# Performance work log

Hardware: AMD Instinct MI355X
Metric: run time of the kernel (lower is better)

The kernel has to match this reference:

```python
import jax, jax.numpy as jnp
import numpy as np

B, T, C = 4, 2048, 1024
H = 16
DH = C // H  # 64


def setup_inputs() -> dict:
    key = jax.random.key(0)
    ks = jax.random.split(key, 6)
    s = 1.0 / np.sqrt(C)
    x = jax.random.normal(ks[0], (B, T, C), dtype=jnp.float32)
    # per-head projection weights, stacked: (H, C, DH)
    Wq = jax.random.uniform(ks[1], (H, C, DH), dtype=jnp.float32, minval=-s, maxval=s)
    Wk = jax.random.uniform(ks[2], (H, C, DH), dtype=jnp.float32, minval=-s, maxval=s)
    Wv = jax.random.uniform(ks[3], (H, C, DH), dtype=jnp.float32, minval=-s, maxval=s)
    # output projection (torch Linear: y = x @ W.T + b); store as (C, C) for x @ Wo
    Wo = jax.random.uniform(ks[4], (C, C), dtype=jnp.float32, minval=-s, maxval=s)
    bo = jax.random.uniform(ks[5], (C,), dtype=jnp.float32, minval=-s, maxval=s)
    return {"x": x, "Wq": Wq, "Wk": Wk, "Wv": Wv, "Wo": Wo, "bo": bo}


def reference(x, Wq, Wk, Wv, Wo, bo):
    # x: (B,T,C) -> q,k,v: (B,H,T,DH)
    q = jnp.einsum('btc,hcd->bhtd', x, Wq)
    k = jnp.einsum('btc,hcd->bhtd', x, Wk)
    v = jnp.einsum('btc,hcd->bhtd', x, Wv)
    scale = DH ** -0.5
    scores = jnp.einsum('bhtd,bhsd->bhts', q, k) * scale  # (B,H,T,T)
    causal = jnp.tril(jnp.ones((T, T), dtype=bool))
    scores = jnp.where(causal, scores, -jnp.inf)
    wei = jax.nn.softmax(scores, axis=-1)
    out = jnp.einsum('bhts,bhsd->bhtd', wei, v)  # (B,H,T,DH)
    # concat heads: (B,T,H*DH) = (B,T,C)
    out = out.transpose(0, 2, 1, 3).reshape(B, T, C)
    return out @ Wo + bo
```

## Files before the change

kernel.cpp:

```cpp
#include <hip/hip_runtime.h>

#define T_SEQ 2048
#define C_DIM 1024
#define H_NUM 16
#define DHD   64
#define B_NUM 4
#define M_ROWS (B_NUM*T_SEQ)

typedef __bf16 bf16x8 __attribute__((ext_vector_type(8)));
typedef float  f32x4  __attribute__((ext_vector_type(4)));
typedef unsigned short ushort8 __attribute__((ext_vector_type(8)));
typedef unsigned short ushort4e __attribute__((ext_vector_type(4)));

__device__ __forceinline__ unsigned short f2b(float f){
  return __builtin_bit_cast(unsigned short, (__bf16)f);
}
__device__ __forceinline__ bf16x8 as_bf(ushort8 u){ return __builtin_bit_cast(bf16x8, u); }
__device__ __forceinline__ float exp2fast(float x){ return __builtin_amdgcn_exp2f(x); }

__device__ __forceinline__ void gload16(const void* g, void* l){
  __builtin_amdgcn_global_load_lds(
      (const __attribute__((address_space(1))) void*)g,
      (__attribute__((address_space(3))) void*)l, 16, 0, 0);
}

#define MF(a,b,c) __builtin_amdgcn_mfma_f32_16x16x32_bf16(a,b,c,0,0,0)

__global__ __launch_bounds__(256) void k_conv_x(const float* __restrict__ x,
                                                unsigned short* __restrict__ xb){
  int i = blockIdx.x*256 + threadIdx.x;
  float4 f = ((const float4*)x)[i];
  ushort4e o;
  o[0]=f2b(f.x); o[1]=f2b(f.y); o[2]=f2b(f.z); o[3]=f2b(f.w);
  ((ushort4e*)xb)[i] = o;
}

__global__ __launch_bounds__(256) void k_pack_w(const float* __restrict__ wq,
                                                const float* __restrict__ wk,
                                                const float* __restrict__ wv,
                                                const float* __restrict__ wo,
                                                unsigned short* __restrict__ wt,
                                                unsigned short* __restrict__ wot){
  int idx = blockIdx.x*256 + threadIdx.x;
  if (idx < 3*C_DIM*C_DIM){
    int nall = idx >> 10; int c = idx & 1023;
    int m = nall >> 10;   int n = nall & 1023;
    int h = n >> 6, d = n & 63;
    const float* w = (m==0) ? wq : (m==1) ? wk : wv;
    float f = w[((size_t)h*C_DIM + c)*DHD + d];
    if (m == 0) f *= 0.125f * 1.4426950408889634f;
    wt[idx] = f2b(f);
  } else {
    int j = idx - 3*C_DIM*C_DIM;
    int n = j >> 10, c = j & 1023;
    wot[j] = f2b(wo[(size_t)c*C_DIM + n]);
  }
}

__global__ __launch_bounds__(256) void k_gemm_qkv(const unsigned short* __restrict__ xb,
                                                  const unsigned short* __restrict__ wt,
                                                  unsigned short* __restrict__ qo,
                                                  unsigned short* __restrict__ ko,
                                                  unsigned short* __restrict__ vo){
  __shared__ __align__(16) unsigned short a_lds[128*64];
  __shared__ __align__(16) unsigned short b_lds[128*64];
  const int tid = threadIdx.x, lane = tid & 63, wid = tid >> 6;
  const int g = lane >> 4, tl = lane & 15;
  const int wr = wid >> 1, wc = wid & 1;
  const int id = blockIdx.x;
  const int swz = (id & 7)*192 + (id >> 3);
  const int mbase = (swz / 24) * 128, nbase = (swz % 24) * 128;
  f32x4 acc[4][4] = {};
  for (int kk = 0; kk < C_DIM; kk += 64){
    __syncthreads();
    #pragma unroll
    for (int i = 0; i < 4; i++){
      const int brow = (wid*4 + i)*8;
      const int row  = brow + (lane >> 3);
      const int jj   = (lane & 7) ^ (row & 7);
      gload16(&xb[(size_t)(mbase+row)*C_DIM + kk + jj*8], &a_lds[brow*64]);
      gload16(&wt[(size_t)(nbase+row)*C_DIM + kk + jj*8], &b_lds[brow*64]);
    }
    __syncthreads();
    bf16x8 aF[4][2], bF[4][2];
    #pragma unroll
    for (int mb = 0; mb < 4; mb++){
      const int row = wr*64 + mb*16 + tl; const int s7 = row & 7;
      aF[mb][0] = as_bf(*(const ushort8*)&a_lds[row*64 + ((g     ^ s7)*8)]);
      aF[mb][1] = as_bf(*(const ushort8*)&a_lds[row*64 + (((4+g) ^ s7)*8)]);
    }
    #pragma unroll
    for (int nb = 0; nb < 4; nb++){
      const int row = wc*64 + nb*16 + tl; const int s7 = row & 7;
      bF[nb][0] = as_bf(*(const ushort8*)&b_lds[row*64 + ((g     ^ s7)*8)]);
      bF[nb][1] = as_bf(*(const ushort8*)&b_lds[row*64 + (((4+g) ^ s7)*8)]);
    }
    #pragma unroll
    for (int mb = 0; mb < 4; mb++)
      #pragma unroll
      for (int nb = 0; nb < 4; nb++){
        acc[mb][nb] = MF(aF[mb][0], bF[nb][0], acc[mb][nb]);
        acc[mb][nb] = MF(aF[mb][1], bF[nb][1], acc[mb][nb]);
      }
  }
  #pragma unroll
  for (int mb = 0; mb < 4; mb++){
    #pragma unroll
    for (int nb = 0; nb < 4; nb++){
      #pragma unroll
      for (int r = 0; r < 4; r++){
        int gr = mbase + wr*64 + mb*16 + g*4 + r;
        int gc = nbase + wc*64 + nb*16 + tl;
        int b = gr >> 11, t = gr & 2047;
        int sel = gc >> 10, nw = gc & 1023;
        int h = nw >> 6, d = nw & 63;
        unsigned short* dst = (sel == 0) ? qo : (sel == 1) ? ko : vo;
        dst[(((size_t)(b*H_NUM + h))*T_SEQ + t)*DHD + d] = f2b(acc[mb][nb][r]);
      }
    }
  }
}

__global__ __launch_bounds__(256) void k_tr_v(const unsigned short* __restrict__ vsrc,
                                              unsigned short* __restrict__ vdst){
  __shared__ __align__(16) unsigned short vr[64][72];
  int tid = threadIdx.x;
  int bh = blockIdx.y; int tbase = blockIdx.x * 64;
  const unsigned short* vb = vsrc + (size_t)bh * T_SEQ * DHD;
  unsigned short* vo = vdst + (size_t)bh * DHD * T_SEQ;
  #pragma unroll
  for (int i = 0; i < 2; i++){
    int id = tid + i*256;
    int row = id >> 3, c8 = (id & 7) << 3;
    *(ushort8*)&vr[row][c8 ^ ((row >> 3) << 3)] =
        *(const ushort8*)&vb[(size_t)(tbase + row)*DHD + c8];
  }
  __syncthreads();
  #pragma unroll
  for (int i = 0; i < 2; i++){
    int id = tid + i*256;
    int d = id >> 3, oc = id & 7;
    ushort8 out;
    #pragma unroll
    for (int j = 0; j < 8; j++){
      int t = oc*8 + j;
      out[j] = vr[t][d ^ (oc << 3)];
    }
    *(ushort8*)&vo[(size_t)d*T_SEQ + tbase + oc*8] = out;
  }
}

__global__ __launch_bounds__(512) void k_flash(const unsigned short* __restrict__ q,
                                               const unsigned short* __restrict__ k,
                                               const unsigned short* __restrict__ vtg,
                                               unsigned short* __restrict__ o){
  __shared__ __align__(16) unsigned short kbufs[2][64*64];
  __shared__ __align__(16) unsigned short vbufs[2][64*64];
  __shared__ __align__(16) unsigned short pl[8][32][72];
  const int tid = threadIdx.x, lane = tid & 63, w = tid >> 6;
  const int g = lane >> 4, tl = lane & 15;
  const int id = blockIdx.x;
  const int swz = (id & 7)*32 + (id >> 3);
  const int bh = swz >> 2, bx = swz & 3;
  const int b = bh >> 4, h = bh & 15;
  const unsigned short* qb = q   + (size_t)bh * T_SEQ * DHD;
  const unsigned short* kb = k   + (size_t)bh * T_SEQ * DHD;
  const unsigned short* vb = vtg + (size_t)bh * (size_t)DHD * T_SEQ;
  const int lrow = lane >> 3, lj = lane & 7;

  for (int pass = 0; pass < 2; ++pass){
    const int qt = pass ? (7 - bx) : bx;
    const int tbase = qt * 256;
    const int trow0 = tbase + w * 32;
    const int tmax = trow0 + 31;
    bf16x8 qF[2][2];
    #pragma unroll
    for (int tf = 0; tf < 2; tf++)
      #pragma unroll
      for (int ks = 0; ks < 2; ks++)
        qF[tf][ks] = as_bf(*(const ushort8*)&qb[(size_t)(trow0 + tf*16 + tl)*DHD + ks*32 + g*8]);
    f32x4 acc[2][4] = {};
    float mreg[2] = {-1e30f, -1e30f}, lreg[2] = {0.f, 0.f};
    const int nkt = 4*qt + 4;
    {
      const int row = w*8 + lrow;
      const int jj = lj ^ (row & 7);
      gload16(&kb[(size_t)row*DHD + jj*8],   &kbufs[0][w*8*64]);
      gload16(&vb[(size_t)row*T_SEQ + jj*8], &vbufs[0][w*8*64]);
    }
    __syncthreads();
    for (int kti = 0; kti < nkt; ++kti){
      const int cur = kti & 1;
      const int kbase = kti * 64;
      if (kti + 1 < nkt){
        const int kb2 = kbase + 64;
        const int row = w*8 + lrow;
        const int jj = lj ^ (row & 7);
        gload16(&kb[(size_t)(kb2+row)*DHD + jj*8],   &kbufs[cur^1][w*8*64]);
        gload16(&vb[(size_t)row*T_SEQ + kb2 + jj*8], &vbufs[cur^1][w*8*64]);
      }
      if (kbase <= tmax){
        const unsigned short* kcur = kbufs[cur];
        const unsigned short* vcur = vbufs[cur];
        const int s7 = tl & 7;
        f32x4 st[2][4] = {};
        __builtin_amdgcn_s_setprio(1);
        #pragma unroll
        for (int sf = 0; sf < 4; sf++){
          const int row = sf*16 + tl;
          bf16x8 kf0 = as_bf(*(const ushort8*)&kcur[row*64 + ((g     ^ s7)*8)]);
          bf16x8 kf1 = as_bf(*(const ushort8*)&kcur[row*64 + (((4+g) ^ s7)*8)]);
          #pragma unroll
          for (int tf = 0; tf < 2; tf++){
            st[tf][sf] = MF(kf0, qF[tf][0], st[tf][sf]);
            st[tf][sf] = MF(kf1, qF[tf][1], st[tf][sf]);
          }
        }
        __builtin_amdgcn_s_setprio(0);
        if (kbase + 63 > trow0){
          #pragma unroll
          for (int tf = 0; tf < 2; tf++){
            int tg = trow0 + tf*16 + tl;
            #pragma unroll
            for (int sf = 0; sf < 4; sf++)
              #pragma unroll
              for (int r = 0; r < 4; r++)
                if (kbase + sf*16 + g*4 + r > tg) st[tf][sf][r] = -1e30f;
          }
        }
        #pragma unroll
        for (int tf = 0; tf < 2; tf++){
          float mloc = -1e30f;
          #pragma unroll
          for (int sf = 0; sf < 4; sf++)
            #pragma unroll
            for (int r = 0; r < 4; r++) mloc = fmaxf(mloc, st[tf][sf][r]);
          if (__any(mloc > mreg[tf] + 8.f)){
            float mrow = fmaxf(mloc, __shfl_xor(mloc, 16));
            mrow = fmaxf(mrow, __shfl_xor(mrow, 32));
            float mnew = fmaxf(mreg[tf], mrow);
            float alpha = exp2fast(mreg[tf] - mnew);
            mreg[tf] = mnew;
            lreg[tf] *= alpha;
            #pragma unroll
            for (int df = 0; df < 4; df++)
              #pragma unroll
              for (int r = 0; r < 4; r++) acc[tf][df][r] *= alpha;
          }
          float sum = 0.f;
          #pragma unroll
          for (int sf = 0; sf < 4; sf++){
            ushort4e pk;
            #pragma unroll
            for (int r = 0; r < 4; r++){
              float p = exp2fast(st[tf][sf][r] - mreg[tf]);
              sum += p;
              pk[r] = f2b(p);
            }
            *(ushort4e*)&pl[w][tf*16 + tl][sf*16 + g*4] = pk;
          }
          lreg[tf] += sum;
        }
        bf16x8 pa[2][2];
        #pragma unroll
        for (int tf = 0; tf < 2; tf++)
          #pragma unroll
          for (int ks = 0; ks < 2; ks++)
            pa[tf][ks] = as_bf(*(const ushort8*)&pl[w][tf*16 + tl][ks*32 + g*8]);
        __builtin_amdgcn_s_setprio(1);
        #pragma unroll
        for (int df = 0; df < 4; df++){
          const int row = df*16 + tl;
          bf16x8 vf0 = as_bf(*(const ushort8*)&vcur[row*64 + ((g     ^ s7)*8)]);
          bf16x8 vf1 = as_bf(*(const ushort8*)&vcur[row*64 + (((4+g) ^ s7)*8)]);
          #pragma unroll
          for (int tf = 0; tf < 2; tf++){
            acc[tf][df] = MF(vf0, pa[tf][0], acc[tf][df]);
            acc[tf][df] = MF(vf1, pa[tf][1], acc[tf][df]);
          }
        }
        __builtin_amdgcn_s_setprio(0);
      }
      __syncthreads();
    }
    #pragma unroll
    for (int tf = 0; tf < 2; tf++){
      float l = lreg[tf];
      l += __shfl_xor(l, 16);
      l += __shfl_xor(l, 32);
      float inv = 1.f / l;
      int tg = trow0 + tf*16 + tl;
      #pragma unroll
      for (int df = 0; df < 4; df++){
        ushort4e ov;
        #pragma unroll
        for (int r = 0; r < 4; r++) ov[r] = f2b(acc[tf][df][r] * inv);
        *(ushort4e*)&o[((size_t)(b*T_SEQ + tg))*C_DIM + h*DHD + df*16 + g*4] = ov;
      }
    }
  }
}

__global__ __launch_bounds__(256) void k_gemm_proj(const unsigned short* __restrict__ ab,
                                                   const unsigned short* __restrict__ wot,
                                                   const float* __restrict__ bo,
                                                   float* __restrict__ out){
  __shared__ __align__(16) unsigned short a_lds[128*64];
  __shared__ __align__(16) unsigned short b_lds[128*64];
  const int tid = threadIdx.x, lane = tid & 63, wid = tid >> 6;
  const int g = lane >> 4, tl = lane & 15;
  const int wr = wid >> 1, wc = wid & 1;
  const int id = blockIdx.x;
  const int swz = (id & 7)*64 + (id >> 3);
  const int mbase = (swz >> 3) * 128, nbase = (swz & 7) * 128;
  f32x4 acc[4][4] = {};
  for (int kk = 0; kk < C_DIM; kk += 64){
    __syncthreads();
    #pragma unroll
    for (int i = 0; i < 4; i++){
      const int brow = (wid*4 + i)*8;
      const int row  = brow + (lane >> 3);
      const int jj   = (lane & 7) ^ (row & 7);
      gload16(&ab[(size_t)(mbase+row)*C_DIM + kk + jj*8],  &a_lds[brow*64]);
      gload16(&wot[(size_t)(nbase+row)*C_DIM + kk + jj*8], &b_lds[brow*64]);
    }
    __syncthreads();
    bf16x8 aF[4][2], bF[4][2];
    #pragma unroll
    for (int mb = 0; mb < 4; mb++){
      const int row = wr*64 + mb*16 + tl; const int s7 = row & 7;
      aF[mb][0] = as_bf(*(const ushort8*)&a_lds[row*64 + ((g     ^ s7)*8)]);
      aF[mb][1] = as_bf(*(const ushort8*)&a_lds[row*64 + (((4+g) ^ s7)*8)]);
    }
    #pragma unroll
    for (int nb = 0; nb < 4; nb++){
      const int row = wc*64 + nb*16 + tl; const int s7 = row & 7;
      bF[nb][0] = as_bf(*(const ushort8*)&b_lds[row*64 + ((g     ^ s7)*8)]);
      bF[nb][1] = as_bf(*(const ushort8*)&b_lds[row*64 + (((4+g) ^ s7)*8)]);
    }
    #pragma unroll
    for (int mb = 0; mb < 4; mb++)
      #pragma unroll
      for (int nb = 0; nb < 4; nb++){
        acc[mb][nb] = MF(aF[mb][0], bF[nb][0], acc[mb][nb]);
        acc[mb][nb] = MF(aF[mb][1], bF[nb][1], acc[mb][nb]);
      }
  }
  #pragma unroll
  for (int mb = 0; mb < 4; mb++){
    #pragma unroll
    for (int nb = 0; nb < 4; nb++){
      #pragma unroll
      for (int r = 0; r < 4; r++){
        int gr = mbase + wr*64 + mb*16 + g*4 + r;
        int gc = nbase + wc*64 + nb*16 + tl;
        out[(size_t)gr*C_DIM + gc] = acc[mb][nb][r] + bo[gc];
      }
    }
  }
}

extern "C" void kernel_launch(void* const* d_in, const int* in_sizes, int n_in,
                              void* d_out, int out_size, void* d_ws, size_t ws_size,
                              hipStream_t stream){
  const float* x  = (const float*)d_in[0];
  const float* Wq = (const float*)d_in[1];
  const float* Wk = (const float*)d_in[2];
  const float* Wv = (const float*)d_in[3];
  const float* Wo = (const float*)d_in[4];
  const float* bo = (const float*)d_in[5];
  float* out = (float*)d_out;

  char* p = (char*)d_ws;
  unsigned short* xb  = (unsigned short*)p; p += (size_t)M_ROWS*C_DIM*2;
  unsigned short* wt  = (unsigned short*)p; p += (size_t)3*C_DIM*C_DIM*2;
  unsigned short* wot = (unsigned short*)p; p += (size_t)C_DIM*C_DIM*2;
  unsigned short* Qb  = (unsigned short*)p; p += (size_t)M_ROWS*C_DIM*2;
  unsigned short* Kb  = (unsigned short*)p; p += (size_t)M_ROWS*C_DIM*2;
  unsigned short* Vb  = (unsigned short*)p; p += (size_t)M_ROWS*C_DIM*2;
  unsigned short* Vtr  = xb;
  unsigned short* attn = Vb;

  hipLaunchKernelGGL(k_conv_x, dim3(M_ROWS*C_DIM/4/256), dim3(256), 0, stream, x, xb);
  hipLaunchKernelGGL(k_pack_w, dim3(4*C_DIM*C_DIM/256), dim3(256), 0, stream,
                     Wq, Wk, Wv, Wo, wt, wot);
  hipLaunchKernelGGL(k_gemm_qkv, dim3(1536), dim3(256), 0, stream,
                     xb, wt, Qb, Kb, Vb);
  hipLaunchKernelGGL(k_tr_v, dim3(T_SEQ/64, B_NUM*H_NUM), dim3(256), 0, stream, Vb, Vtr);
  hipLaunchKernelGGL(k_flash, dim3(256), dim3(512), 0, stream,
                     Qb, Kb, Vtr, attn);
  hipLaunchKernelGGL(k_gemm_proj, dim3(512), dim3(256), 0, stream,
                     attn, wot, bo, out);
}
```

Before: 185.3 us.

## Merge prep kernels and enlarge GEMM tiles to 256x128 with 8 waves

```diff
diff --git a/kernel.cpp b/kernel.cpp
--- a/kernel.cpp
+++ b/kernel.cpp
@@ -26,72 +26,80 @@
 
 #define MF(a,b,c) __builtin_amdgcn_mfma_f32_16x16x32_bf16(a,b,c,0,0,0)
 
-__global__ __launch_bounds__(256) void k_conv_x(const float* __restrict__ x,
-                                                unsigned short* __restrict__ xb){
-  int i = blockIdx.x*256 + threadIdx.x;
-  float4 f = ((const float4*)x)[i];
-  ushort4e o;
-  o[0]=f2b(f.x); o[1]=f2b(f.y); o[2]=f2b(f.z); o[3]=f2b(f.w);
-  ((ushort4e*)xb)[i] = o;
-}
-
-__global__ __launch_bounds__(256) void k_pack_w(const float* __restrict__ wq,
-                                                const float* __restrict__ wk,
-                                                const float* __restrict__ wv,
-                                                const float* __restrict__ wo,
-                                                unsigned short* __restrict__ wt,
-                                                unsigned short* __restrict__ wot){
-  int idx = blockIdx.x*256 + threadIdx.x;
-  if (idx < 3*C_DIM*C_DIM){
-    int nall = idx >> 10; int c = idx & 1023;
-    int m = nall >> 10;   int n = nall & 1023;
-    int h = n >> 6, d = n & 63;
-    const float* w = (m==0) ? wq : (m==1) ? wk : wv;
-    float f = w[((size_t)h*C_DIM + c)*DHD + d];
-    if (m == 0) f *= 0.125f * 1.4426950408889634f;
-    wt[idx] = f2b(f);
+__global__ __launch_bounds__(256) void k_prep(const float* __restrict__ x,
+                                              const float* __restrict__ wq,
+                                              const float* __restrict__ wk,
+                                              const float* __restrict__ wv,
+                                              const float* __restrict__ wo,
+                                              unsigned short* __restrict__ xb,
+                                              unsigned short* __restrict__ wt,
+                                              unsigned short* __restrict__ wot){
+  const int bid = blockIdx.x;
+  if (bid < 8192){
+    int i = bid*256 + threadIdx.x;
+    float4 f = ((const float4*)x)[i];
+    ushort4e o;
+    o[0]=f2b(f.x); o[1]=f2b(f.y); o[2]=f2b(f.z); o[3]=f2b(f.w);
+    ((ushort4e*)xb)[i] = o;
   } else {
-    int j = idx - 3*C_DIM*C_DIM;
-    int n = j >> 10, c = j & 1023;
-    wot[j] = f2b(wo[(size_t)c*C_DIM + n]);
-  }
-}
-
-__global__ __launch_bounds__(256) void k_gemm_qkv(const unsigned short* __restrict__ xb,
-                                                  const unsigned short* __restrict__ wt,
-                                                  unsigned short* __restrict__ qo,
-                                                  unsigned short* __restrict__ ko,
-                                                  unsigned short* __restrict__ vo){
-  __shared__ __align__(16) unsigned short a_lds[128*64];
+    int idx = (bid - 8192)*256 + threadIdx.x;
+    if (idx < 3*C_DIM*C_DIM){
+      int nall = idx >> 10; int c = idx & 1023;
+      int m = nall >> 10;   int n = nall & 1023;
+      int h = n >> 6, d = n & 63;
+      const float* w = (m==0) ? wq : (m==1) ? wk : wv;
+      float f = w[((size_t)h*C_DIM + c)*DHD + d];
+      if (m == 0) f *= 0.125f * 1.4426950408889634f;
+      wt[idx] = f2b(f);
+    } else {
+      int j = idx - 3*C_DIM*C_DIM;
+      int n = j >> 10, c = j & 1023;
+      wot[j] = f2b(wo[(size_t)c*C_DIM + n]);
+    }
+  }
+}
+
+__global__ __launch_bounds__(512, 4) void k_gemm_qkv(const unsigned short* __restrict__ xb,
+                                                     const unsigned short* __restrict__ wt,
+                                                     unsigned short* __restrict__ qo,
+                                                     unsigned short* __restrict__ ko,
+                                                     unsigned short* __restrict__ vo){
+  __shared__ __align__(16) unsigned short a_lds[256*64];
   __shared__ __align__(16) unsigned short b_lds[128*64];
   const int tid = threadIdx.x, lane = tid & 63, wid = tid >> 6;
   const int g = lane >> 4, tl = lane & 15;
-  const int wr = wid >> 1, wc = wid & 1;
+  const int wm = wid >> 1, wn = wid & 1;
+  const int wmb = wm*64, wnb = wn*64;
   const int id = blockIdx.x;
-  const int swz = (id & 7)*192 + (id >> 3);
-  const int mbase = (swz / 24) * 128, nbase = (swz % 24) * 128;
+  const int swz = (id & 7)*96 + (id >> 3);
+  const int mbase = (swz / 24) * 256, nbase = (swz % 24) * 128;
+  const int srow = tid >> 3;
+  const int jj   = (((tid & 7) ^ (srow & 7)) * 8);
+  const int jdst = (tid & 7) * 8;
   f32x4 acc[4][4] = {};
   for (int kk = 0; kk < C_DIM; kk += 64){
     __syncthreads();
     #pragma unroll
     for (int i = 0; i < 4; i++){
-      const int brow = (wid*4 + i)*8;
-      const int row  = brow + (lane >> 3);
-      const int jj   = (lane & 7) ^ (row & 7);
-      gload16(&xb[(size_t)(mbase+row)*C_DIM + kk + jj*8], &a_lds[brow*64]);
-      gload16(&wt[(size_t)(nbase+row)*C_DIM + kk + jj*8], &b_lds[brow*64]);
+      const int row = i*64 + srow;
+      gload16(&xb[(size_t)(mbase+row)*C_DIM + kk + jj], &a_lds[row*64 + jdst]);
+    }
+    #pragma unroll
+    for (int i = 0; i < 2; i++){
+      const int row = i*64 + srow;
+      gload16(&wt[(size_t)(nbase+row)*C_DIM + kk + jj], &b_lds[row*64 + jdst]);
     }
     __syncthreads();
     bf16x8 aF[4][2], bF[4][2];
     #pragma unroll
     for (int mb = 0; mb < 4; mb++){
-      const int row = wr*64 + mb*16 + tl; const int s7 = row & 7;
+      const int row = wmb + mb*16 + tl; const int s7 = row & 7;
       aF[mb][0] = as_bf(*(const ushort8*)&a_lds[row*64 + ((g     ^ s7)*8)]);
       aF[mb][1] = as_bf(*(const ushort8*)&a_lds[row*64 + (((4+g) ^ s7)*8)]);
     }
     #pragma unroll
     for (int nb = 0; nb < 4; nb++){
-      const int row = wc*64 + nb*16 + tl; const int s7 = row & 7;
+      const int row = wnb + nb*16 + tl; const int s7 = row & 7;
       bF[nb][0] = as_bf(*(const ushort8*)&b_lds[row*64 + ((g     ^ s7)*8)]);
       bF[nb][1] = as_bf(*(const ushort8*)&b_lds[row*64 + (((4+g) ^ s7)*8)]);
     }
@@ -109,8 +117,8 @@
     for (int nb = 0; nb < 4; nb++){
       #pragma unroll
       for (int r = 0; r < 4; r++){
-        int gr = mbase + wr*64 + mb*16 + g*4 + r;
-        int gc = nbase + wc*64 + nb*16 + tl;
+        int gr = mbase + wmb + mb*16 + g*4 + r;
+        int gc = nbase + wnb + nb*16 + tl;
         int b = gr >> 11, t = gr & 2047;
         int sel = gc >> 10, nw = gc & 1023;
         int h = nw >> 6, d = nw & 63;
@@ -301,40 +309,46 @@
   }
 }
 
-__global__ __launch_bounds__(256) void k_gemm_proj(const unsigned short* __restrict__ ab,
-                                                   const unsigned short* __restrict__ wot,
-                                                   const float* __restrict__ bo,
-                                                   float* __restrict__ out){
-  __shared__ __align__(16) unsigned short a_lds[128*64];
+__global__ __launch_bounds__(512, 4) void k_gemm_proj(const unsigned short* __restrict__ ab,
+                                                      const unsigned short* __restrict__ wot,
+                                                      const float* __restrict__ bo,
+                                                      float* __restrict__ out){
+  __shared__ __align__(16) unsigned short a_lds[256*64];
   __shared__ __align__(16) unsigned short b_lds[128*64];
   const int tid = threadIdx.x, lane = tid & 63, wid = tid >> 6;
   const int g = lane >> 4, tl = lane & 15;
-  const int wr = wid >> 1, wc = wid & 1;
+  const int wm = wid >> 1, wn = wid & 1;
+  const int wmb = wm*64, wnb = wn*64;
   const int id = blockIdx.x;
-  const int swz = (id & 7)*64 + (id >> 3);
-  const int mbase = (swz >> 3) * 128, nbase = (swz & 7) * 128;
+  const int swz = (id & 7)*32 + (id >> 3);
+  const int mbase = (swz >> 3) * 256, nbase = (swz & 7) * 128;
+  const int srow = tid >> 3;
+  const int jj   = (((tid & 7) ^ (srow & 7)) * 8);
+  const int jdst = (tid & 7) * 8;
   f32x4 acc[4][4] = {};
   for (int kk = 0; kk < C_DIM; kk += 64){
     __syncthreads();
     #pragma unroll
     for (int i = 0; i < 4; i++){
-      const int brow = (wid*4 + i)*8;
-      const int row  = brow + (lane >> 3);
-      const int jj   = (lane & 7) ^ (row & 7);
-      gload16(&ab[(size_t)(mbase+row)*C_DIM + kk + jj*8],  &a_lds[brow*64]);
-      gload16(&wot[(size_t)(nbase+row)*C_DIM + kk + jj*8], &b_lds[brow*64]);
+      const int row = i*64 + srow;
+      gload16(&ab[(size_t)(mbase+row)*C_DIM + kk + jj], &a_lds[row*64 + jdst]);
+    }
+    #pragma unroll
+    for (int i = 0; i < 2; i++){
+      const int row = i*64 + srow;
+      gload16(&wot[(size_t)(nbase+row)*C_DIM + kk + jj], &b_lds[row*64 + jdst]);
     }
     __syncthreads();
     bf16x8 aF[4][2], bF[4][2];
     #pragma unroll
     for (int mb = 0; mb < 4; mb++){
-      const int row = wr*64 + mb*16 + tl; const int s7 = row & 7;
+      const int row = wmb + mb*16 + tl; const int s7 = row & 7;
       aF[mb][0] = as_bf(*(const ushort8*)&a_lds[row*64 + ((g     ^ s7)*8)]);
       aF[mb][1] = as_bf(*(const ushort8*)&a_lds[row*64 + (((4+g) ^ s7)*8)]);
     }
     #pragma unroll
     for (int nb = 0; nb < 4; nb++){
-      const int row = wc*64 + nb*16 + tl; const int s7 = row & 7;
+      const int row = wnb + nb*16 + tl; const int s7 = row & 7;
       bF[nb][0] = as_bf(*(const ushort8*)&b_lds[row*64 + ((g     ^ s7)*8)]);
       bF[nb][1] = as_bf(*(const ushort8*)&b_lds[row*64 + (((4+g) ^ s7)*8)]);
     }
@@ -352,8 +366,8 @@
     for (int nb = 0; nb < 4; nb++){
       #pragma unroll
       for (int r = 0; r < 4; r++){
-        int gr = mbase + wr*64 + mb*16 + g*4 + r;
-        int gc = nbase + wc*64 + nb*16 + tl;
+        int gr = mbase + wmb + mb*16 + g*4 + r;
+        int gc = nbase + wnb + nb*16 + tl;
         out[(size_t)gr*C_DIM + gc] = acc[mb][nb][r] + bo[gc];
       }
     }
@@ -381,14 +395,13 @@
   unsigned short* Vtr  = xb;
   unsigned short* attn = Vb;
 
-  hipLaunchKernelGGL(k_conv_x, dim3(M_ROWS*C_DIM/4/256), dim3(256), 0, stream, x, xb);
-  hipLaunchKernelGGL(k_pack_w, dim3(4*C_DIM*C_DIM/256), dim3(256), 0, stream,
-                     Wq, Wk, Wv, Wo, wt, wot);
-  hipLaunchKernelGGL(k_gemm_qkv, dim3(1536), dim3(256), 0, stream,
+  hipLaunchKernelGGL(k_prep, dim3(8192 + 16384), dim3(256), 0, stream,
+                     x, Wq, Wk, Wv, Wo, xb, wt, wot);
+  hipLaunchKernelGGL(k_gemm_qkv, dim3(768), dim3(512), 0, stream,
                      xb, wt, Qb, Kb, Vb);
   hipLaunchKernelGGL(k_tr_v, dim3(T_SEQ/64, B_NUM*H_NUM), dim3(256), 0, stream, Vb, Vtr);
   hipLaunchKernelGGL(k_flash, dim3(256), dim3(512), 0, stream,
                      Qb, Kb, Vtr, attn);
-  hipLaunchKernelGGL(k_gemm_proj, dim3(512), dim3(256), 0, stream,
+  hipLaunchKernelGGL(k_gemm_proj, dim3(256), dim3(512), 0, stream,
                      attn, wot, bo, out);
 }
```

Measured after the change: 202.6 us. 1.09x slower.
